# Kernel tuning notes

Measured on AMD Instinct MI355X. Metric: run time of the kernel, lower is better.

The kernel has to match this reference:

```python
import jax, jax.numpy as jnp
import numpy as np

IN_DIM = 300
MEM_DIM = 1024
DEPTH = 14  # perfect binary tree in heap order: N = 2**DEPTH - 1 = 16383 nodes


def _init_linear(key, out_dim, in_dim):
    # torch nn.Linear default init: U(-1/sqrt(in), 1/sqrt(in)) for W and b
    s = 1.0 / np.sqrt(in_dim)
    kw, kb = jax.random.split(key)
    W = jax.random.uniform(kw, (out_dim, in_dim), jnp.float32, -s, s)
    b = jax.random.uniform(kb, (out_dim,), jnp.float32, -s, s)
    return W, b


def setup_inputs() -> dict:
    key = jax.random.key(0)
    keys = jax.random.split(key, 9)
    N = 2 ** DEPTH - 1
    inp = {"embs": jax.random.normal(keys[0], (N, IN_DIM), jnp.float32)}
    gates = [("ix", IN_DIM), ("ih", MEM_DIM), ("fx", IN_DIM), ("fh", MEM_DIM),
             ("ox", IN_DIM), ("oh", MEM_DIM), ("ux", IN_DIM), ("uh", MEM_DIM)]
    for k, (name, d) in zip(keys[1:], gates):
        W, b = _init_linear(k, MEM_DIM, d)
        inp["W" + name] = W
        inp["b" + name] = b
    inp["depth"] = DEPTH
    return inp


def _lin(x, W, b):
    return x @ W.T + b


def reference(embs, Wix, bix, Wih, bih, Wfx, bfx, Wfh, bfh,
              Wox, box, Woh, boh, Wux, bux, Wuh, buh, depth):
    # Child-Sum TreeLSTM on a perfect binary tree (heap order), processed
    # bottom-up, batching all nodes of a level into single GEMMs.
    h = c = None
    for lvl in range(depth - 1, -1, -1):
        n = 2 ** lvl
        x = embs[n - 1:2 * n - 1]  # [n, in_dim], nodes of this level
        if h is None:
            # leaves: original code feeds a single zero child -> h_sum = 0
            # and f * child_c = 0 regardless of f
            hsum = jnp.zeros((n, MEM_DIM), embs.dtype)
            fc = jnp.zeros((n, MEM_DIM), embs.dtype)
        else:
            hc = h.reshape(n, 2, MEM_DIM)  # children hidden states
            cc = c.reshape(n, 2, MEM_DIM)  # children cell states
            hsum = hc.sum(axis=1)
            # per-child forget gate: sigmoid(fh(h_k) + fx(x))
            f = jax.nn.sigmoid(jnp.einsum('nkd,md->nkm', hc, Wfh) + bfh
                               + _lin(x, Wfx, bfx)[:, None, :])
            fc = (f * cc).sum(axis=1)
        i = jax.nn.sigmoid(_lin(x, Wix, bix) + _lin(hsum, Wih, bih))
        o = jax.nn.sigmoid(_lin(x, Wox, box) + _lin(hsum, Woh, boh))
        u = jnp.tanh(_lin(x, Wux, bux) + _lin(hsum, Wuh, buh))
        c = i * u + fc
        h = o * jnp.tanh(c)
    return jnp.stack([c[0], h[0]])  # root state (c, h): [2, MEM_DIM]
```

## Files before the change

kernel.cpp:

```cpp
#include <hip/hip_runtime.h>
#include <hip/hip_bf16.h>

#define IN_DIM 300
#define XDIM   320
#define MEM    1024
#define NTREE  16383

typedef _Float16 half8 __attribute__((ext_vector_type(8)));
typedef float    f32x4 __attribute__((ext_vector_type(4)));

__device__ __forceinline__ float sigf(float x) { return 1.0f / (1.0f + __expf(-x)); }
__device__ __forceinline__ float tanhfast(float x) { return 2.0f / (1.0f + __expf(-2.0f * x)) - 1.0f; }

#define GLOAD_LDS16(g, l) \
    __builtin_amdgcn_global_load_lds((const __attribute__((address_space(1))) void*)(g), \
                                     (__attribute__((address_space(3))) void*)(l), 16, 0, 0)

__global__ void pack_kernel(
    const float* __restrict__ embs,
    const float* __restrict__ Wix, const float* __restrict__ bix,
    const float* __restrict__ Wih, const float* __restrict__ bih,
    const float* __restrict__ Wfx, const float* __restrict__ bfx,
    const float* __restrict__ Wfh, const float* __restrict__ bfh,
    const float* __restrict__ Wox, const float* __restrict__ box_,
    const float* __restrict__ Woh, const float* __restrict__ boh,
    const float* __restrict__ Wux, const float* __restrict__ bux,
    const float* __restrict__ Wuh, const float* __restrict__ buh,
    _Float16* __restrict__ Wiou16, _Float16* __restrict__ Wfh16,
    _Float16* __restrict__ x16, _Float16* __restrict__ Bx)
{
    long long idx = (long long)blockIdx.x * blockDim.x + threadIdx.x;
    const long long n_wiou = 3072LL * 1024;
    const long long n_wfh  = 1024LL * 1024;
    const long long n_x    = 16384LL * XDIM;
    const long long n_bx   = 4096LL * XDIM;
    if (idx < n_wiou) {
        int m = (int)(idx >> 10), k = (int)(idx & 1023);
        int g = m >> 10, mm = m & 1023;
        const float* W = (g == 0) ? Wih : (g == 1) ? Woh : Wuh;
        Wiou16[idx] = (_Float16)W[(long long)mm * MEM + k];
        return;
    }
    idx -= n_wiou;
    if (idx < n_wfh) {
        Wfh16[idx] = (_Float16)Wfh[idx];
        return;
    }
    idx -= n_wfh;
    if (idx < n_x) {
        int node = (int)(idx / XDIM), j = (int)(idx % XDIM);
        float v = 0.f;
        if (node < NTREE) {
            if (j < IN_DIM) v = embs[(long long)node * IN_DIM + j];
            else if (j == IN_DIM) v = 1.0f;
        }
        x16[idx] = (_Float16)v;
        return;
    }
    idx -= n_x;
    if (idx < n_bx) {
        int r = (int)(idx / XDIM), j = (int)(idx % XDIM);
        int g = r >> 10, mm = r & 1023;
        const float* Wx = (g == 0) ? Wix : (g == 1) ? Wox : (g == 2) ? Wux : Wfx;
        const float* b1 = (g == 0) ? bix : (g == 1) ? box_ : (g == 2) ? bux : bfx;
        const float* b2 = (g == 0) ? bih : (g == 1) ? boh : (g == 2) ? buh : bfh;
        float v = 0.f;
        if (j < IN_DIM) v = Wx[(long long)mm * IN_DIM + j];
        else if (j == IN_DIM) v = b1[mm] + b2[mm];
        Bx[idx] = (_Float16)v;
    }
}

template<int BM, int BN, int BK>
__device__ __forceinline__ void gemm_core(
    const _Float16* __restrict__ A, int lda,
    const _Float16* __restrict__ B, int ldb, int K,
    _Float16* ldsA, _Float16* ldsB,
    f32x4 (&acc)[BM / 32][BN / 32])
{
    constexpr int FM = BM / 32, FN = BN / 32;
    constexpr int CPR = BK / 8, SWM = CPR - 1;
    constexpr int ACH = BM * BK / 2048, BCH = BN * BK / 2048;

    int tid = threadIdx.x, wave = tid >> 6, lane = tid & 63;
    int wr = (wave >> 1) * (BM / 2), wc = (wave & 1) * (BN / 2);
    int kq = (lane >> 4) * 8, rs = lane & 15;

    for (int k0 = 0; k0 < K; k0 += BK) {
#pragma unroll
        for (int j = 0; j < ACH; ++j) {
            int c = j * 256 + tid;
            int row = c / CPR;
            int s = (c ^ row) & SWM;
            GLOAD_LDS16(A + (long long)row * lda + k0 + s * 8,
                        &ldsA[(j * 256 + wave * 64) * 8]);
        }
#pragma unroll
        for (int j = 0; j < BCH; ++j) {
            int c = j * 256 + tid;
            int row = c / CPR;
            int s = (c ^ row) & SWM;
            GLOAD_LDS16(B + (long long)row * ldb + k0 + s * 8,
                        &ldsB[(j * 256 + wave * 64) * 8]);
        }
        __syncthreads();
#pragma unroll
        for (int kk = 0; kk < BK; kk += 32) {
            half8 a[FM], b[FN];
#pragma unroll
            for (int i = 0; i < FM; ++i) {
                int r = wr + i * 16 + rs;
                int s = ((kk + kq) >> 3) ^ (r & SWM);
                a[i] = *(const half8*)&ldsA[r * BK + s * 8];
            }
#pragma unroll
            for (int i = 0; i < FN; ++i) {
                int r = wc + i * 16 + rs;
                int s = ((kk + kq) >> 3) ^ (r & SWM);
                b[i] = *(const half8*)&ldsB[r * BK + s * 8];
            }
#pragma unroll
            for (int mi = 0; mi < FM; ++mi)
#pragma unroll
                for (int ni = 0; ni < FN; ++ni)
                    acc[mi][ni] = __builtin_amdgcn_mfma_f32_16x16x32_f16(a[mi], b[ni], acc[mi][ni], 0, 0, 0);
        }
        __syncthreads();
    }
}

__global__ __launch_bounds__(256) void proj_fused(
    const _Float16* __restrict__ x16, const _Float16* __restrict__ Bx,
    _Float16* __restrict__ Xp,
    _Float16* __restrict__ cleaf, _Float16* __restrict__ hleaf,
    _Float16* __restrict__ hsum)
{
    __shared__ __align__(16) _Float16 lds[448 * 32];
    int tid = threadIdx.x, wave = tid >> 6, lane = tid & 63;
    int kq = (lane >> 4) * 8, rs = lane & 15;

    if (blockIdx.x < 2048) {
        int mb = blockIdx.x & 63, nb = blockIdx.x >> 6;
        f32x4 acc[4][4] = {};
        gemm_core<128, 128, 32>(x16 + (long long)mb * 128 * XDIM, XDIM,
                                Bx + (long long)nb * 128 * XDIM, XDIM, XDIM,
                                lds, lds + 4096, acc);
        int wr = (wave >> 1) * 64, wc = (wave & 1) * 64;
        int crb = wr + (lane >> 4) * 4, ccb = wc + rs;
#pragma unroll
        for (int mi = 0; mi < 4; ++mi)
#pragma unroll
            for (int i = 0; i < 4; ++i) {
                long long r = mb * 128 + crb + mi * 16 + i;
#pragma unroll
                for (int ni = 0; ni < 4; ++ni)
                    Xp[r * 4096 + nb * 128 + ccb + ni * 16] = (_Float16)acc[mi][ni][i];
            }
        return;
    }
    {
        constexpr int BK = 32, CPR = 4, SWM = 3;
        _Float16* lA = lds;
        _Float16* lB = lds + 64 * 32;
        int bid = (int)blockIdx.x - 2048;
        int m0 = (bid & 127) * 64, c0 = (bid >> 7) * 128;
        int wr = (wave >> 1) * 32, wc = (wave & 1) * 64;
        const _Float16* A = x16 + (size_t)(8191 + m0) * XDIM;

        f32x4 acc[3][2][4] = {};
        for (int t = 0; t < 10; ++t) {
            int k0 = t * BK;
            {
                int c = tid, row = c / CPR, s = (c ^ row) & SWM;
                GLOAD_LDS16(A + (long long)row * XDIM + k0 + s * 8, &lA[(wave * 64) * 8]);
            }
#pragma unroll
            for (int j = 0; j < 6; ++j) {
                int c = j * 256 + tid;
                int row = c / CPR, s = (c ^ row) & SWM;
                int g = row >> 7, rr = row & 127;
                GLOAD_LDS16(Bx + (long long)(g * 1024 + c0 + rr) * XDIM + k0 + s * 8,
                            &lB[(j * 256 + wave * 64) * 8]);
            }
            __syncthreads();
            half8 a[2], b[3][4];
#pragma unroll
            for (int mi = 0; mi < 2; ++mi) {
                int r = wr + mi * 16 + rs;
                int s = (kq >> 3) ^ (r & SWM);
                a[mi] = *(const half8*)&lA[r * BK + s * 8];
            }
#pragma unroll
            for (int g = 0; g < 3; ++g)
#pragma unroll
                for (int nj = 0; nj < 4; ++nj) {
                    int r = g * 128 + wc + nj * 16 + rs;
                    int s = (kq >> 3) ^ (r & SWM);
                    b[g][nj] = *(const half8*)&lB[r * BK + s * 8];
                }
#pragma unroll
            for (int g = 0; g < 3; ++g)
#pragma unroll
                for (int mi = 0; mi < 2; ++mi)
#pragma unroll
                    for (int nj = 0; nj < 4; ++nj)
                        acc[g][mi][nj] = __builtin_amdgcn_mfma_f32_16x16x32_f16(a[mi], b[g][nj], acc[g][mi][nj], 0, 0, 0);
            __syncthreads();
        }
        int lrb = wr + (lane >> 4) * 4;
#pragma unroll
        for (int mi = 0; mi < 2; ++mi)
#pragma unroll
            for (int nj = 0; nj < 4; ++nj) {
                int col = c0 + wc + nj * 16 + rs;
                float hpair = 0.f;
#pragma unroll
                for (int i = 0; i < 4; ++i) {
                    long long l = m0 + lrb + mi * 16 + i;
                    float cc = sigf(acc[0][mi][nj][i]) * tanhfast(acc[2][mi][nj][i]);
                    float hh = sigf(acc[1][mi][nj][i]) * tanhfast(cc);
                    cleaf[l * 1024 + col] = (_Float16)cc;
                    hleaf[l * 1024 + col] = (_Float16)hh;
                    if (i & 1) hsum[(l >> 1) * 1024 + col] = (_Float16)(hpair + hh);
                    else hpair = hh;
                }
            }
    }
}

template<int BM1, int BM2, int BK>
__global__ __launch_bounds__(256) void gemm_level_act(
    const _Float16* __restrict__ Hsum, const _Float16* __restrict__ Hc,
    const _Float16* __restrict__ Wiou, const _Float16* __restrict__ Wf,
    const _Float16* __restrict__ Xp,
    _Float16* __restrict__ houact, _Float16* __restrict__ fact,
    int G1, int G2, int n)
{
    constexpr int BMX = (BM1 > BM2) ? BM1 : BM2;
    __shared__ __align__(16) _Float16 ldsA[BMX * BK];
    __shared__ __align__(16) _Float16 ldsB[128 * BK];
    int tid = threadIdx.x, wave = tid >> 6, lane = tid & 63;
    int bx = blockIdx.x;
    if (bx < G1 * 24) {
        int nb = bx / G1, mb = bx % G1;
        f32x4 acc[BM1 / 32][4] = {};
        gemm_core<BM1, 128, BK>(Hsum + (long long)mb * BM1 * 1024, 1024,
                                Wiou + (long long)nb * 128 * 1024, 1024, 1024,
                                ldsA, ldsB, acc);
        int gate = nb >> 3;
        int wr = (wave >> 1) * (BM1 / 2), wc = (wave & 1) * 64;
        int crb = wr + (lane >> 4) * 4, ccb = wc + (lane & 15);
#pragma unroll
        for (int mi = 0; mi < BM1 / 32; ++mi)
#pragma unroll
            for (int i = 0; i < 4; ++i) {
                long long row = mb * BM1 + crb + mi * 16 + i;
                long long node = (n - 1) + row;
#pragma unroll
                for (int ni = 0; ni < 4; ++ni) {
                    int col = nb * 128 + ccb + ni * 16;
                    float v = acc[mi][ni][i] + (float)Xp[node * 4096 + col];
                    float a = (gate == 2) ? tanhfast(v) : sigf(v);
                    houact[row * 3072 + col] = (_Float16)a;
                }
            }
    } else {
        int b2 = bx - G1 * 24;
        int nb = b2 / G2, mb = b2 % G2;
        f32x4 acc[BM2 / 32][4] = {};
        gemm_core<BM2, 128, BK>(Hc + (long long)mb * BM2 * 1024, 1024,
                                Wf + (long long)nb * 128 * 1024, 1024, 1024,
                                ldsA, ldsB, acc);
        int wr = (wave >> 1) * (BM2 / 2), wc = (wave & 1) * 64;
        int crb = wr + (lane >> 4) * 4, ccb = wc + (lane & 15);
#pragma unroll
        for (int mi = 0; mi < BM2 / 32; ++mi)
#pragma unroll
            for (int i = 0; i < 4; ++i) {
                long long row = mb * BM2 + crb + mi * 16 + i;
                long long node = (n - 1) + (row >> 1);
#pragma unroll
                for (int ni = 0; ni < 4; ++ni) {
                    int col = nb * 128 + ccb + ni * 16;
                    float v = acc[mi][ni][i] + (float)Xp[node * 4096 + 3072 + col];
                    fact[row * 1024 + col] = (_Float16)sigf(v);
                }
            }
    }
}

template<bool C16>
__global__ void combine_act(
    const _Float16* __restrict__ houact, const _Float16* __restrict__ fact,
    const void* __restrict__ cprevp,
    float* __restrict__ cout, _Float16* __restrict__ hout, _Float16* __restrict__ hsum,
    int n)
{
    int idx = blockIdx.x * blockDim.x + threadIdx.x;
    int npairs = n >> 1;
    if (idx >= npairs * 128) return;
    int r = idx >> 7, m8 = (idx & 127) * 8;
    float hs[8];
#pragma unroll
    for (int j = 0; j < 8; ++j) hs[j] = 0.f;
    for (int t = 0; t < 2; ++t) {
        int p = 2 * r + t;
        half8 vi = *(const half8*)&houact[(long long)p * 3072 + m8];
        half8 vo = *(const half8*)&houact[(long long)p * 3072 + 1024 + m8];
        half8 vu = *(const half8*)&houact[(long long)p * 3072 + 2048 + m8];
        half8 f0 = *(const half8*)&fact[(long long)(2 * p) * 1024 + m8];
        half8 f1 = *(const half8*)&fact[(long long)(2 * p + 1) * 1024 + m8];
        float c0[8], c1[8];
        if (C16) {
            const _Float16* cp = (const _Float16*)cprevp;
            half8 a = *(const half8*)&cp[(long long)(2 * p) * 1024 + m8];
            half8 b = *(const half8*)&cp[(long long)(2 * p + 1) * 1024 + m8];
#pragma unroll
            for (int j = 0; j < 8; ++j) { c0[j] = (float)a[j]; c1[j] = (float)b[j]; }
        } else {
            const float* cp = (const float*)cprevp;
            f32x4 a0 = *(const f32x4*)&cp[(long long)(2 * p) * 1024 + m8];
            f32x4 a1 = *(const f32x4*)&cp[(long long)(2 * p) * 1024 + m8 + 4];
            f32x4 b0 = *(const f32x4*)&cp[(long long)(2 * p + 1) * 1024 + m8];
            f32x4 b1 = *(const f32x4*)&cp[(long long)(2 * p + 1) * 1024 + m8 + 4];
#pragma unroll
            for (int j = 0; j < 4; ++j) { c0[j] = a0[j]; c0[j + 4] = a1[j]; c1[j] = b0[j]; c1[j + 4] = b1[j]; }
        }
        float cw[8], hw[8];
#pragma unroll
        for (int j = 0; j < 8; ++j) {
            float c = (float)vi[j] * (float)vu[j]
                    + (float)f0[j] * c0[j] + (float)f1[j] * c1[j];
            float h = (float)vo[j] * tanhfast(c);
            cw[j] = c; hw[j] = h; hs[j] += h;
        }
        f32x4 v0 = {cw[0], cw[1], cw[2], cw[3]}, v1 = {cw[4], cw[5], cw[6], cw[7]};
        *(f32x4*)&cout[(long long)p * 1024 + m8] = v0;
        *(f32x4*)&cout[(long long)p * 1024 + m8 + 4] = v1;
        half8 hv;
#pragma unroll
        for (int j = 0; j < 8; ++j) hv[j] = (_Float16)hw[j];
        *(half8*)&hout[(long long)p * 1024 + m8] = hv;
    }
    half8 sv;
#pragma unroll
    for (int j = 0; j < 8; ++j) sv[j] = (_Float16)hs[j];
    *(half8*)&hsum[(long long)r * 1024 + m8] = sv;
}

__global__ __launch_bounds__(256) void tail_sk(
    const _Float16* __restrict__ Hs, const _Float16* __restrict__ Hc,
    const _Float16* __restrict__ Wiou, const _Float16* __restrict__ Wf,
    float* __restrict__ houp, float* __restrict__ fp,
    int n, int PTn, int PT2n)
{
    __shared__ __align__(16) _Float16 ldsA[64 * 128];
    __shared__ __align__(16) _Float16 ldsB[128 * 128];
    int tid = threadIdx.x, wave = tid >> 6, lane = tid & 63;
    int T = PTn * 24 + PT2n * 8;
    int s = blockIdx.x / T, r = blockIdx.x % T;
    int k0 = s * 256;
    f32x4 acc[2][4] = {};
    int wr = (wave >> 1) * 32, wc = (wave & 1) * 64;
    int crb = wr + (lane >> 4) * 4, ccb = wc + (lane & 15);
    if (r < PTn * 24) {
        int nb = r / PTn, mb = r % PTn;
        gemm_core<64, 128, 128>(Hs + (long long)mb * 64 * 1024 + k0, 1024,
                                Wiou + (long long)nb * 128 * 1024 + k0, 1024, 256,
                                ldsA, ldsB, acc);
#pragma unroll
        for (int mi = 0; mi < 2; ++mi)
#pragma unroll
            for (int i = 0; i < 4; ++i) {
                int row = mb * 64 + crb + mi * 16 + i;
                if (row >= n) continue;
#pragma unroll
                for (int ni = 0; ni < 4; ++ni)
                    houp[((long long)s * n + row) * 3072 + nb * 128 + ccb + ni * 16] = acc[mi][ni][i];
            }
    } else {
        int b2 = r - PTn * 24;
        int nb = b2 / PT2n, mb = b2 % PT2n;
        gemm_core<64, 128, 128>(Hc + (long long)mb * 64 * 1024 + k0, 1024,
                                Wf + (long long)nb * 128 * 1024 + k0, 1024, 256,
                                ldsA, ldsB, acc);
#pragma unroll
        for (int mi = 0; mi < 2; ++mi)
#pragma unroll
            for (int i = 0; i < 4; ++i) {
                int row = mb * 64 + crb + mi * 16 + i;
                if (row >= 2 * n) continue;
#pragma unroll
                for (int ni = 0; ni < 4; ++ni)
                    fp[((long long)s * 2 * n + row) * 1024 + nb * 128 + ccb + ni * 16] = acc[mi][ni][i];
            }
    }
}

__global__ void combine_tail(
    const float* __restrict__ houp, const float* __restrict__ fp,
    const float* __restrict__ cprev, const _Float16* __restrict__ Xp,
    float* __restrict__ cout, _Float16* __restrict__ hout, _Float16* __restrict__ hsum,
    int n, float* __restrict__ fin)
{
    int idx = blockIdx.x * blockDim.x + threadIdx.x;
    int npairs = (n > 1) ? (n >> 1) : 1;
    if (idx >= npairs * 128) return;
    int r = idx >> 7, m8 = (idx & 127) * 8;
    float hs[8];
#pragma unroll
    for (int j = 0; j < 8; ++j) hs[j] = 0.f;
    int pmax = (n > 1) ? 2 : 1;
    for (int t = 0; t < pmax; ++t) {
        int p = 2 * r + t;
        long long node = (n - 1) + p;
        float gi[8], go[8], gu[8], q0[8], q1[8];
        half8 xi = *(const half8*)&Xp[node * 4096 + m8];
        half8 xo = *(const half8*)&Xp[node * 4096 + 1024 + m8];
        half8 xu = *(const half8*)&Xp[node * 4096 + 2048 + m8];
        half8 xf = *(const half8*)&Xp[node * 4096 + 3072 + m8];
#pragma unroll
        for (int j = 0; j < 8; ++j) {
            gi[j] = (float)xi[j]; go[j] = (float)xo[j]; gu[j] = (float)xu[j];
            q0[j] = (float)xf[j]; q1[j] = (float)xf[j];
        }
#pragma unroll
        for (int s = 0; s < 4; ++s) {
            const float* hb = houp + ((long long)s * n + p) * 3072;
#pragma unroll
            for (int j = 0; j < 8; ++j) {
                gi[j] += hb[m8 + j];
                go[j] += hb[1024 + m8 + j];
                gu[j] += hb[2048 + m8 + j];
            }
            const float* fb0 = fp + ((long long)s * 2 * n + 2 * p) * 1024;
            const float* fb1 = fp + ((long long)s * 2 * n + 2 * p + 1) * 1024;
#pragma unroll
            for (int j = 0; j < 8; ++j) {
                q0[j] += fb0[m8 + j];
                q1[j] += fb1[m8 + j];
            }
        }
        float cw[8], hw[8];
#pragma unroll
        for (int j = 0; j < 8; ++j) {
            float i  = sigf(gi[j]);
            float o  = sigf(go[j]);
            float u  = tanhfast(gu[j]);
            float f0 = sigf(q0[j]);
            float f1 = sigf(q1[j]);
            float c = i * u + f0 * cprev[(long long)(2 * p) * 1024 + m8 + j]
                            + f1 * cprev[(long long)(2 * p + 1) * 1024 + m8 + j];
            float h = o * tanhfast(c);
            cw[j] = c; hw[j] = h; hs[j] += h;
        }
        if (fin) {
            f32x4 v0 = {cw[0], cw[1], cw[2], cw[3]}, v1 = {cw[4], cw[5], cw[6], cw[7]};
            f32x4 w0 = {hw[0], hw[1], hw[2], hw[3]}, w1 = {hw[4], hw[5], hw[6], hw[7]};
            *(f32x4*)&fin[m8] = v0;            *(f32x4*)&fin[m8 + 4] = v1;
            *(f32x4*)&fin[1024 + m8] = w0;     *(f32x4*)&fin[1024 + m8 + 4] = w1;
        } else {
            f32x4 v0 = {cw[0], cw[1], cw[2], cw[3]}, v1 = {cw[4], cw[5], cw[6], cw[7]};
            *(f32x4*)&cout[(long long)p * 1024 + m8] = v0;
            *(f32x4*)&cout[(long long)p * 1024 + m8 + 4] = v1;
            half8 hv;
#pragma unroll
            for (int j = 0; j < 8; ++j) hv[j] = (_Float16)hw[j];
            *(half8*)&hout[(long long)p * 1024 + m8] = hv;
        }
    }
    if (!fin) {
        half8 sv;
#pragma unroll
        for (int j = 0; j < 8; ++j) sv[j] = (_Float16)hs[j];
        *(half8*)&hsum[(long long)r * 1024 + m8] = sv;
    }
}

extern "C" void kernel_launch(void* const* d_in, const int* in_sizes, int n_in,
                              void* d_out, int out_size, void* d_ws, size_t ws_size,
                              hipStream_t stream)
{
    const float* embs = (const float*)d_in[0];
    const float* Wix = (const float*)d_in[1];  const float* bix = (const float*)d_in[2];
    const float* Wih = (const float*)d_in[3];  const float* bih = (const float*)d_in[4];
    const float* Wfx = (const float*)d_in[5];  const float* bfx = (const float*)d_in[6];
    const float* Wfh = (const float*)d_in[7];  const float* bfh = (const float*)d_in[8];
    const float* Wox = (const float*)d_in[9];  const float* box_ = (const float*)d_in[10];
    const float* Woh = (const float*)d_in[11]; const float* boh = (const float*)d_in[12];
    const float* Wux = (const float*)d_in[13]; const float* bux = (const float*)d_in[14];
    const float* Wuh = (const float*)d_in[15]; const float* buh = (const float*)d_in[16];

    char* p = (char*)d_ws;
    auto carve = [&](size_t bytes) -> char* {
        char* r = p; p += (bytes + 255) & ~(size_t)255; return r;
    };
    _Float16* Wiou16 = (_Float16*)carve((size_t)3072 * 1024 * 2);
    _Float16* Wfh16  = (_Float16*)carve((size_t)1024 * 1024 * 2);
    _Float16* Xp     = (_Float16*)carve((size_t)8192 * 4096 * 2);
    _Float16* houact = (_Float16*)carve((size_t)4096 * 3072 * 2);
    _Float16* fact   = (_Float16*)carve((size_t)8192 * 1024 * 2);
    _Float16* H_A    = (_Float16*)carve((size_t)8192 * 1024 * 2);
    _Float16* H_B    = (_Float16*)carve((size_t)4096 * 1024 * 2);
    _Float16* HsumA  = (_Float16*)carve((size_t)4096 * 1024 * 2);
    _Float16* HsumB  = (_Float16*)carve((size_t)4096 * 1024 * 2);
    _Float16* Cleaf  = (_Float16*)carve((size_t)8192 * 1024 * 2);
    float*    Cping  = (float*)carve((size_t)4096 * 1024 * 4);
    float*    Cpong  = (float*)carve((size_t)2048 * 1024 * 4);
    float*    houp4  = (float*)carve((size_t)4 * 256 * 3072 * 4);
    float*    fp4    = (float*)carve((size_t)4 * 512 * 1024 * 4);
    _Float16* x16 = fact;
    _Float16* Bx  = fact + (size_t)16384 * XDIM;

    {
        long long tot = 3072LL * 1024 + 1024LL * 1024 + 16384LL * XDIM + 4096LL * XDIM;
        pack_kernel<<<dim3((int)((tot + 255) / 256)), dim3(256), 0, stream>>>(
            embs, Wix, bix, Wih, bih, Wfx, bfx, Wfh, bfh,
            Wox, box_, Woh, boh, Wux, bux, Wuh, buh,
            Wiou16, Wfh16, x16, Bx);
    }

    proj_fused<<<dim3(3072), dim3(256), 0, stream>>>(
        x16, Bx, Xp, Cleaf, H_A, HsumA);

    const void* cprev = Cleaf;
    float* cbufs[2] = {Cping, Cpong};
    _Float16* hsums[2] = {HsumA, HsumB};
    int ci = 0, si = 0;
    _Float16* hcur = H_A;
    _Float16* hnext = H_B;

    for (int lvl = 12; lvl >= 9; --lvl) {
        int n = 1 << lvl;
        int G1 = n / 128, G2 = 2 * n / 128;
        if (n >= 1024)
            gemm_level_act<128, 128, 32><<<dim3(G1 * 24 + G2 * 8), dim3(256), 0, stream>>>(
                hsums[si], hcur, Wiou16, Wfh16, Xp, houact, fact, G1, G2, n);
        else
            gemm_level_act<128, 128, 128><<<dim3(G1 * 24 + G2 * 8), dim3(256), 0, stream>>>(
                hsums[si], hcur, Wiou16, Wfh16, Xp, houact, fact, G1, G2, n);
        int blocks = ((n >> 1) * 128 + 255) / 256;
        if (lvl == 12)
            combine_act<true><<<dim3(blocks), dim3(256), 0, stream>>>(
                houact, fact, cprev, cbufs[ci], hnext, hsums[si ^ 1], n);
        else
            combine_act<false><<<dim3(blocks), dim3(256), 0, stream>>>(
                houact, fact, cprev, cbufs[ci], hnext, hsums[si ^ 1], n);
        cprev = cbufs[ci];
        ci ^= 1; si ^= 1;
        _Float16* tmp = hcur; hcur = hnext; hnext = tmp;
    }

    for (int lvl = 8; lvl >= 0; --lvl) {
        int n = 1 << lvl;
        int PTn = (n + 63) / 64, PT2n = (2 * n + 63) / 64;
        int T = PTn * 24 + PT2n * 8;
        tail_sk<<<dim3(T * 4), dim3(256), 0, stream>>>(
            hsums[si], hcur, Wiou16, Wfh16, houp4, fp4, n, PTn, PT2n);
        int npairs = (n > 1) ? (n >> 1) : 1;
        int blocks = (npairs * 128 + 255) / 256;
        combine_tail<<<dim3(blocks), dim3(256), 0, stream>>>(
            houp4, fp4, (const float*)cprev, Xp,
            cbufs[ci], hnext, hsums[si ^ 1], n,
            (lvl == 0) ? (float*)d_out : nullptr);
        cprev = cbufs[ci];
        ci ^= 1; si ^= 1;
        _Float16* tmp = hcur; hcur = hnext; hnext = tmp;
    }
}
```

Before: 474.2 us.

## Replace split-K tail GEMMs with full-K level GEMMs and split fused projection

Result: slower. 487.4 us (+2.8%).

```diff
diff --git a/kernel.cpp b/kernel.cpp
--- a/kernel.cpp
+++ b/kernel.cpp
@@ -129,103 +129,32 @@
     }
 }
 
-__global__ __launch_bounds__(256) void proj_fused(
-    const _Float16* __restrict__ x16, const _Float16* __restrict__ Bx,
-    _Float16* __restrict__ Xp,
-    _Float16* __restrict__ cleaf, _Float16* __restrict__ hleaf,
-    _Float16* __restrict__ hsum)
-{
-    __shared__ __align__(16) _Float16 lds[448 * 32];
+template<int BM, int BN, int BK>
+__global__ __launch_bounds__(256) void gemm_f16(
+    const _Float16* __restrict__ A, int lda,
+    const _Float16* __restrict__ B, int ldb,
+    _Float16* __restrict__ C, int ldc, int K)
+{
+    __shared__ __align__(16) _Float16 ldsA[BM * BK];
+    __shared__ __align__(16) _Float16 ldsB[BN * BK];
+    constexpr int FM = BM / 32, FN = BN / 32;
+    f32x4 acc[FM][FN] = {};
+    gemm_core<BM, BN, BK>(A + (long long)blockIdx.x * BM * lda, lda,
+                          B + (long long)blockIdx.y * BN * ldb, ldb, K,
+                          ldsA, ldsB, acc);
     int tid = threadIdx.x, wave = tid >> 6, lane = tid & 63;
-    int kq = (lane >> 4) * 8, rs = lane & 15;
-
-    if (blockIdx.x < 2048) {
-        int mb = blockIdx.x & 63, nb = blockIdx.x >> 6;
-        f32x4 acc[4][4] = {};
-        gemm_core<128, 128, 32>(x16 + (long long)mb * 128 * XDIM, XDIM,
-                                Bx + (long long)nb * 128 * XDIM, XDIM, XDIM,
-                                lds, lds + 4096, acc);
-        int wr = (wave >> 1) * 64, wc = (wave & 1) * 64;
-        int crb = wr + (lane >> 4) * 4, ccb = wc + rs;
-#pragma unroll
-        for (int mi = 0; mi < 4; ++mi)
-#pragma unroll
-            for (int i = 0; i < 4; ++i) {
-                long long r = mb * 128 + crb + mi * 16 + i;
-#pragma unroll
-                for (int ni = 0; ni < 4; ++ni)
-                    Xp[r * 4096 + nb * 128 + ccb + ni * 16] = (_Float16)acc[mi][ni][i];
-            }
-        return;
-    }
-    {
-        constexpr int BK = 32, CPR = 4, SWM = 3;
-        _Float16* lA = lds;
-        _Float16* lB = lds + 64 * 32;
-        int bid = (int)blockIdx.x - 2048;
-        int m0 = (bid & 127) * 64, c0 = (bid >> 7) * 128;
-        int wr = (wave >> 1) * 32, wc = (wave & 1) * 64;
-        const _Float16* A = x16 + (size_t)(8191 + m0) * XDIM;
-
-        f32x4 acc[3][2][4] = {};
-        for (int t = 0; t < 10; ++t) {
-            int k0 = t * BK;
-            {
-                int c = tid, row = c / CPR, s = (c ^ row) & SWM;
-                GLOAD_LDS16(A + (long long)row * XDIM + k0 + s * 8, &lA[(wave * 64) * 8]);
-            }
-#pragma unroll
-            for (int j = 0; j < 6; ++j) {
-                int c = j * 256 + tid;
-                int row = c / CPR, s = (c ^ row) & SWM;
-                int g = row >> 7, rr = row & 127;
-                GLOAD_LDS16(Bx + (long long)(g * 1024 + c0 + rr) * XDIM + k0 + s * 8,
-                            &lB[(j * 256 + wave * 64) * 8]);
-            }
-            __syncthreads();
-            half8 a[2], b[3][4];
-#pragma unroll
-            for (int mi = 0; mi < 2; ++mi) {
-                int r = wr + mi * 16 + rs;
-                int s = (kq >> 3) ^ (r & SWM);
-                a[mi] = *(const half8*)&lA[r * BK + s * 8];
-            }
-#pragma unroll
-            for (int g = 0; g < 3; ++g)
-#pragma unroll
-                for (int nj = 0; nj < 4; ++nj) {
-                    int r = g * 128 + wc + nj * 16 + rs;
-                    int s = (kq >> 3) ^ (r & SWM);
-                    b[g][nj] = *(const half8*)&lB[r * BK + s * 8];
-                }
-#pragma unroll
-            for (int g = 0; g < 3; ++g)
-#pragma unroll
-                for (int mi = 0; mi < 2; ++mi)
-#pragma unroll
-                    for (int nj = 0; nj < 4; ++nj)
-                        acc[g][mi][nj] = __builtin_amdgcn_mfma_f32_16x16x32_f16(a[mi], b[g][nj], acc[g][mi][nj], 0, 0, 0);
-            __syncthreads();
-        }
-        int lrb = wr + (lane >> 4) * 4;
-#pragma unroll
-        for (int mi = 0; mi < 2; ++mi)
-#pragma unroll
-            for (int nj = 0; nj < 4; ++nj) {
-                int col = c0 + wc + nj * 16 + rs;
-                float hpair = 0.f;
-#pragma unroll
-                for (int i = 0; i < 4; ++i) {
-                    long long l = m0 + lrb + mi * 16 + i;
-                    float cc = sigf(acc[0][mi][nj][i]) * tanhfast(acc[2][mi][nj][i]);
-                    float hh = sigf(acc[1][mi][nj][i]) * tanhfast(cc);
-                    cleaf[l * 1024 + col] = (_Float16)cc;
-                    hleaf[l * 1024 + col] = (_Float16)hh;
-                    if (i & 1) hsum[(l >> 1) * 1024 + col] = (_Float16)(hpair + hh);
-                    else hpair = hh;
-                }
-            }
-    }
+    int wr = (wave >> 1) * (BM / 2), wc = (wave & 1) * (BN / 2);
+    int crb = wr + (lane >> 4) * 4, ccb = wc + (lane & 15);
+    long long m0 = (long long)blockIdx.x * BM, n0 = (long long)blockIdx.y * BN;
+#pragma unroll
+    for (int mi = 0; mi < FM; ++mi)
+#pragma unroll
+        for (int i = 0; i < 4; ++i) {
+            long long r = m0 + crb + mi * 16 + i;
+#pragma unroll
+            for (int ni = 0; ni < FN; ++ni)
+                C[r * ldc + n0 + ccb + ni * 16] = (_Float16)acc[mi][ni][i];
+        }
 }
 
 template<int BM1, int BM2, int BK>
@@ -348,60 +277,136 @@
     *(half8*)&hsum[(long long)r * 1024 + m8] = sv;
 }
 
-__global__ __launch_bounds__(256) void tail_sk(
-    const _Float16* __restrict__ Hs, const _Float16* __restrict__ Hc,
+__global__ __launch_bounds__(256) void leaf_fused(
+    const _Float16* __restrict__ x16, const _Float16* __restrict__ Bx,
+    _Float16* __restrict__ cleaf, _Float16* __restrict__ hleaf,
+    _Float16* __restrict__ hsum)
+{
+    constexpr int BK = 32, CPR = 4, SWM = 3;
+    __shared__ __align__(16) _Float16 lA[64 * BK];
+    __shared__ __align__(16) _Float16 lB[384 * BK];
+    int tid = threadIdx.x, wave = tid >> 6, lane = tid & 63;
+    int kq = (lane >> 4) * 8, rs = lane & 15;
+    int wr = (wave >> 1) * 32, wc = (wave & 1) * 64;
+    int m0 = blockIdx.x * 64, c0 = blockIdx.y * 128;
+    const _Float16* A = x16 + (size_t)(8191 + m0) * XDIM;
+
+    f32x4 acc[3][2][4] = {};
+    for (int t = 0; t < 10; ++t) {
+        int k0 = t * BK;
+        {
+            int c = tid, row = c / CPR, s = (c ^ row) & SWM;
+            GLOAD_LDS16(A + (long long)row * XDIM + k0 + s * 8, &lA[(wave * 64) * 8]);
+        }
+#pragma unroll
+        for (int j = 0; j < 6; ++j) {
+            int c = j * 256 + tid;
+            int row = c / CPR, s = (c ^ row) & SWM;
+            int g = row >> 7, rr = row & 127;
+            GLOAD_LDS16(Bx + (long long)(g * 1024 + c0 + rr) * XDIM + k0 + s * 8,
+                        &lB[(j * 256 + wave * 64) * 8]);
+        }
+        __syncthreads();
+        half8 a[2], b[3][4];
+#pragma unroll
+        for (int mi = 0; mi < 2; ++mi) {
+            int r = wr + mi * 16 + rs;
+            int s = (kq >> 3) ^ (r & SWM);
+            a[mi] = *(const half8*)&lA[r * BK + s * 8];
+        }
+#pragma unroll
+        for (int g = 0; g < 3; ++g)
+#pragma unroll
+            for (int nj = 0; nj < 4; ++nj) {
+                int r = g * 128 + wc + nj * 16 + rs;
+                int s = (kq >> 3) ^ (r & SWM);
+                b[g][nj] = *(const half8*)&lB[r * BK + s * 8];
+            }
+#pragma unroll
+        for (int g = 0; g < 3; ++g)
+#pragma unroll
+            for (int mi = 0; mi < 2; ++mi)
+#pragma unroll
+                for (int nj = 0; nj < 4; ++nj)
+                    acc[g][mi][nj] = __builtin_amdgcn_mfma_f32_16x16x32_f16(a[mi], b[g][nj], acc[g][mi][nj], 0, 0, 0);
+        __syncthreads();
+    }
+    int lrb = wr + (lane >> 4) * 4;
+#pragma unroll
+    for (int mi = 0; mi < 2; ++mi)
+#pragma unroll
+        for (int nj = 0; nj < 4; ++nj) {
+            int col = c0 + wc + nj * 16 + rs;
+            float hpair = 0.f;
+#pragma unroll
+            for (int i = 0; i < 4; ++i) {
+                long long l = m0 + lrb + mi * 16 + i;
+                float cc = sigf(acc[0][mi][nj][i]) * tanhfast(acc[2][mi][nj][i]);
+                float hh = sigf(acc[1][mi][nj][i]) * tanhfast(cc);
+                cleaf[l * 1024 + col] = (_Float16)cc;
+                hleaf[l * 1024 + col] = (_Float16)hh;
+                if (i & 1) hsum[(l >> 1) * 1024 + col] = (_Float16)(hpair + hh);
+                else hpair = hh;
+            }
+        }
+}
+
+template<int BM1, int BM2, int BK>
+__global__ __launch_bounds__(256) void gemm_level(
+    const _Float16* __restrict__ Hsum, const _Float16* __restrict__ Hc,
     const _Float16* __restrict__ Wiou, const _Float16* __restrict__ Wf,
-    float* __restrict__ houp, float* __restrict__ fp,
-    int n, int PTn, int PT2n)
-{
-    __shared__ __align__(16) _Float16 ldsA[64 * 128];
-    __shared__ __align__(16) _Float16 ldsB[128 * 128];
+    _Float16* __restrict__ houpre, _Float16* __restrict__ fpre,
+    int G1, int G2)
+{
+    constexpr int BMX = (BM1 > BM2) ? BM1 : BM2;
+    __shared__ __align__(16) _Float16 ldsA[BMX * BK];
+    __shared__ __align__(16) _Float16 ldsB[128 * BK];
     int tid = threadIdx.x, wave = tid >> 6, lane = tid & 63;
-    int T = PTn * 24 + PT2n * 8;
-    int s = blockIdx.x / T, r = blockIdx.x % T;
-    int k0 = s * 256;
-    f32x4 acc[2][4] = {};
-    int wr = (wave >> 1) * 32, wc = (wave & 1) * 64;
-    int crb = wr + (lane >> 4) * 4, ccb = wc + (lane & 15);
-    if (r < PTn * 24) {
-        int nb = r / PTn, mb = r % PTn;
-        gemm_core<64, 128, 128>(Hs + (long long)mb * 64 * 1024 + k0, 1024,
-                                Wiou + (long long)nb * 128 * 1024 + k0, 1024, 256,
+    int bx = blockIdx.x;
+    if (bx < G1 * 24) {
+        int nb = bx / G1, mb = bx % G1;
+        f32x4 acc[BM1 / 32][4] = {};
+        gemm_core<BM1, 128, BK>(Hsum + (long long)mb * BM1 * 1024, 1024,
+                                Wiou + (long long)nb * 128 * 1024, 1024, 1024,
                                 ldsA, ldsB, acc);
-#pragma unroll
-        for (int mi = 0; mi < 2; ++mi)
+        int wr = (wave >> 1) * (BM1 / 2), wc = (wave & 1) * 64;
+        int crb = wr + (lane >> 4) * 4, ccb = wc + (lane & 15);
+#pragma unroll
+        for (int mi = 0; mi < BM1 / 32; ++mi)
 #pragma unroll
             for (int i = 0; i < 4; ++i) {
-                int row = mb * 64 + crb + mi * 16 + i;
-                if (row >= n) continue;
+                long long row = mb * BM1 + crb + mi * 16 + i;
 #pragma unroll
                 for (int ni = 0; ni < 4; ++ni)
-                    houp[((long long)s * n + row) * 3072 + nb * 128 + ccb + ni * 16] = acc[mi][ni][i];
+                    houpre[row * 3072 + nb * 128 + ccb + ni * 16] = (_Float16)acc[mi][ni][i];
             }
     } else {
-        int b2 = r - PTn * 24;
-        int nb = b2 / PT2n, mb = b2 % PT2n;
-        gemm_core<64, 128, 128>(Hc + (long long)mb * 64 * 1024 + k0, 1024,
-                                Wf + (long long)nb * 128 * 1024 + k0, 1024, 256,
+        int b2 = bx - G1 * 24;
+        int nb = b2 / G2, mb = b2 % G2;
+        f32x4 acc[BM2 / 32][4] = {};
+        gemm_core<BM2, 128, BK>(Hc + (long long)mb * BM2 * 1024, 1024,
+                                Wf + (long long)nb * 128 * 1024, 1024, 1024,
                                 ldsA, ldsB, acc);
-#pragma unroll
-        for (int mi = 0; mi < 2; ++mi)
+        int wr = (wave >> 1) * (BM2 / 2), wc = (wave & 1) * 64;
+        int crb = wr + (lane >> 4) * 4, ccb = wc + (lane & 15);
+#pragma unroll
+        for (int mi = 0; mi < BM2 / 32; ++mi)
 #pragma unroll
             for (int i = 0; i < 4; ++i) {
-                int row = mb * 64 + crb + mi * 16 + i;
-                if (row >= 2 * n) continue;
+                long long row = mb * BM2 + crb + mi * 16 + i;
 #pragma unroll
                 for (int ni = 0; ni < 4; ++ni)
-                    fp[((long long)s * 2 * n + row) * 1024 + nb * 128 + ccb + ni * 16] = acc[mi][ni][i];
-            }
-    }
-}
-
-__global__ void combine_tail(
-    const float* __restrict__ houp, const float* __restrict__ fp,
-    const float* __restrict__ cprev, const _Float16* __restrict__ Xp,
+                    fpre[row * 1024 + nb * 128 + ccb + ni * 16] = (_Float16)acc[mi][ni][i];
+            }
+    }
+}
+
+__global__ void combine_level(
+    const _Float16* __restrict__ houpre, const _Float16* __restrict__ fpre,
+    const float* __restrict__ cprev,
+    const _Float16* __restrict__ Xp,
     float* __restrict__ cout, _Float16* __restrict__ hout, _Float16* __restrict__ hsum,
-    int n, float* __restrict__ fin)
+    int n, int gx0, float* __restrict__ fin)
 {
     int idx = blockIdx.x * blockDim.x + threadIdx.x;
     int npairs = (n > 1) ? (n >> 1) : 1;
@@ -413,42 +418,24 @@
     int pmax = (n > 1) ? 2 : 1;
     for (int t = 0; t < pmax; ++t) {
         int p = 2 * r + t;
-        long long node = (n - 1) + p;
-        float gi[8], go[8], gu[8], q0[8], q1[8];
-        half8 xi = *(const half8*)&Xp[node * 4096 + m8];
-        half8 xo = *(const half8*)&Xp[node * 4096 + 1024 + m8];
-        half8 xu = *(const half8*)&Xp[node * 4096 + 2048 + m8];
-        half8 xf = *(const half8*)&Xp[node * 4096 + 3072 + m8];
+        long long node = gx0 + p;
+        half8 phi = *(const half8*)&houpre[(long long)p * 3072 + m8];
+        half8 pho = *(const half8*)&houpre[(long long)p * 3072 + 1024 + m8];
+        half8 phu = *(const half8*)&houpre[(long long)p * 3072 + 2048 + m8];
+        half8 pxi = *(const half8*)&Xp[node * 4096 + m8];
+        half8 pxo = *(const half8*)&Xp[node * 4096 + 1024 + m8];
+        half8 pxu = *(const half8*)&Xp[node * 4096 + 2048 + m8];
+        half8 pxf = *(const half8*)&Xp[node * 4096 + 3072 + m8];
+        half8 pf0 = *(const half8*)&fpre[(long long)(2 * p) * 1024 + m8];
+        half8 pf1 = *(const half8*)&fpre[(long long)(2 * p + 1) * 1024 + m8];
+        float cw[8], hw[8];
 #pragma unroll
         for (int j = 0; j < 8; ++j) {
-            gi[j] = (float)xi[j]; go[j] = (float)xo[j]; gu[j] = (float)xu[j];
-            q0[j] = (float)xf[j]; q1[j] = (float)xf[j];
-        }
-#pragma unroll
-        for (int s = 0; s < 4; ++s) {
-            const float* hb = houp + ((long long)s * n + p) * 3072;
-#pragma unroll
-            for (int j = 0; j < 8; ++j) {
-                gi[j] += hb[m8 + j];
-                go[j] += hb[1024 + m8 + j];
-                gu[j] += hb[2048 + m8 + j];
-            }
-            const float* fb0 = fp + ((long long)s * 2 * n + 2 * p) * 1024;
-            const float* fb1 = fp + ((long long)s * 2 * n + 2 * p + 1) * 1024;
-#pragma unroll
-            for (int j = 0; j < 8; ++j) {
-                q0[j] += fb0[m8 + j];
-                q1[j] += fb1[m8 + j];
-            }
-        }
-        float cw[8], hw[8];
-#pragma unroll
-        for (int j = 0; j < 8; ++j) {
-            float i  = sigf(gi[j]);
-            float o  = sigf(go[j]);
-            float u  = tanhfast(gu[j]);
-            float f0 = sigf(q0[j]);
-            float f1 = sigf(q1[j]);
+            float i  = sigf((float)phi[j] + (float)pxi[j]);
+            float o  = sigf((float)pho[j] + (float)pxo[j]);
+            float u  = tanhfast((float)phu[j] + (float)pxu[j]);
+            float f0 = sigf((float)pf0[j] + (float)pxf[j]);
+            float f1 = sigf((float)pf1[j] + (float)pxf[j]);
             float c = i * u + f0 * cprev[(long long)(2 * p) * 1024 + m8 + j]
                             + f1 * cprev[(long long)(2 * p + 1) * 1024 + m8 + j];
             float h = o * tanhfast(c);
@@ -498,8 +485,8 @@
     _Float16* Wiou16 = (_Float16*)carve((size_t)3072 * 1024 * 2);
     _Float16* Wfh16  = (_Float16*)carve((size_t)1024 * 1024 * 2);
     _Float16* Xp     = (_Float16*)carve((size_t)8192 * 4096 * 2);
-    _Float16* houact = (_Float16*)carve((size_t)4096 * 3072 * 2);
-    _Float16* fact   = (_Float16*)carve((size_t)8192 * 1024 * 2);
+    _Float16* houpre = (_Float16*)carve((size_t)4096 * 3072 * 2);
+    _Float16* fpre   = (_Float16*)carve((size_t)8192 * 1024 * 2);
     _Float16* H_A    = (_Float16*)carve((size_t)8192 * 1024 * 2);
     _Float16* H_B    = (_Float16*)carve((size_t)4096 * 1024 * 2);
     _Float16* HsumA  = (_Float16*)carve((size_t)4096 * 1024 * 2);
@@ -507,10 +494,8 @@
     _Float16* Cleaf  = (_Float16*)carve((size_t)8192 * 1024 * 2);
     float*    Cping  = (float*)carve((size_t)4096 * 1024 * 4);
     float*    Cpong  = (float*)carve((size_t)2048 * 1024 * 4);
-    float*    houp4  = (float*)carve((size_t)4 * 256 * 3072 * 4);
-    float*    fp4    = (float*)carve((size_t)4 * 512 * 1024 * 4);
-    _Float16* x16 = fact;
-    _Float16* Bx  = fact + (size_t)16384 * XDIM;
+    _Float16* x16 = fpre;
+    _Float16* Bx  = fpre + (size_t)16384 * XDIM;
 
     {
         long long tot = 3072LL * 1024 + 1024LL * 1024 + 16384LL * XDIM + 4096LL * XDIM;
@@ -520,8 +505,9 @@
             Wiou16, Wfh16, x16, Bx);
     }
 
-    proj_fused<<<dim3(3072), dim3(256), 0, stream>>>(
-        x16, Bx, Xp, Cleaf, H_A, HsumA);
+    gemm_f16<128, 128, 32><<<dim3(64, 32), dim3(256), 0, stream>>>(
+        x16, XDIM, Bx, XDIM, Xp, 4096, XDIM);
+    leaf_fused<<<dim3(128, 8), dim3(256), 0, stream>>>(x16, Bx, Cleaf, H_A, HsumA);
 
     const void* cprev = Cleaf;
     float* cbufs[2] = {Cping, Cpong};
@@ -535,17 +521,17 @@
         int G1 = n / 128, G2 = 2 * n / 128;
         if (n >= 1024)
             gemm_level_act<128, 128, 32><<<dim3(G1 * 24 + G2 * 8), dim3(256), 0, stream>>>(
-                hsums[si], hcur, Wiou16, Wfh16, Xp, houact, fact, G1, G2, n);
+                hsums[si], hcur, Wiou16, Wfh16, Xp, houpre, fpre, G1, G2, n);
         else
             gemm_level_act<128, 128, 128><<<dim3(G1 * 24 + G2 * 8), dim3(256), 0, stream>>>(
-                hsums[si], hcur, Wiou16, Wfh16, Xp, houact, fact, G1, G2, n);
+                hsums[si], hcur, Wiou16, Wfh16, Xp, houpre, fpre, G1, G2, n);
         int blocks = ((n >> 1) * 128 + 255) / 256;
         if (lvl == 12)
             combine_act<true><<<dim3(blocks), dim3(256), 0, stream>>>(
-                houact, fact, cprev, cbufs[ci], hnext, hsums[si ^ 1], n);
+                houpre, fpre, cprev, cbufs[ci], hnext, hsums[si ^ 1], n);
         else
             combine_act<false><<<dim3(blocks), dim3(256), 0, stream>>>(
-                houact, fact, cprev, cbufs[ci], hnext, hsums[si ^ 1], n);
+                houpre, fpre, cprev, cbufs[ci], hnext, hsums[si ^ 1], n);
         cprev = cbufs[ci];
         ci ^= 1; si ^= 1;
         _Float16* tmp = hcur; hcur = hnext; hnext = tmp;
@@ -553,15 +539,22 @@
 
     for (int lvl = 8; lvl >= 0; --lvl) {
         int n = 1 << lvl;
-        int PTn = (n + 63) / 64, PT2n = (2 * n + 63) / 64;
-        int T = PTn * 24 + PT2n * 8;
-        tail_sk<<<dim3(T * 4), dim3(256), 0, stream>>>(
-            hsums[si], hcur, Wiou16, Wfh16, houp4, fp4, n, PTn, PT2n);
+        if (n >= 128) {
+            int G1 = n / 128, G2 = 2 * n / 128;
+            gemm_level<128, 128, 128><<<dim3(G1 * 24 + G2 * 8), dim3(256), 0, stream>>>(
+                hsums[si], hcur, Wiou16, Wfh16, houpre, fpre, G1, G2);
+        } else if (n == 64) {
+            gemm_level<64, 128, 128><<<dim3(32), dim3(256), 0, stream>>>(
+                hsums[si], hcur, Wiou16, Wfh16, houpre, fpre, 1, 1);
+        } else {
+            gemm_level<64, 64, 128><<<dim3(32), dim3(256), 0, stream>>>(
+                hsums[si], hcur, Wiou16, Wfh16, houpre, fpre, 1, 1);
+        }
         int npairs = (n > 1) ? (n >> 1) : 1;
         int blocks = (npairs * 128 + 255) / 256;
-        combine_tail<<<dim3(blocks), dim3(256), 0, stream>>>(
-            houp4, fp4, (const float*)cprev, Xp,
-            cbufs[ci], hnext, hsums[si ^ 1], n,
+        combine_level<<<dim3(blocks), dim3(256), 0, stream>>>(
+            houpre, fpre, (const float*)cprev, Xp,
+            cbufs[ci], hnext, hsums[si ^ 1], n, n - 1,
             (lvl == 0) ? (float*)d_out : nullptr);
         cprev = cbufs[ci];
         ci ^= 1; si ^= 1;
```
